# Performance work log

Hardware: AMD Instinct MI355X
Metric: run time of the kernel (lower is better)

## Reference

```python
import jax, jax.numpy as jnp
import numpy as np

D, U, NNZ, B = 8192, 4096, 1_700_000, 1024

def setup_inputs() -> dict:
    key = jax.random.key(0)
    k1, k2, k3, k4 = jax.random.split(key, 4)
    x = jax.random.normal(k1, (B, D), dtype=jnp.float32)
    kernel_vector = jax.random.normal(k2, (NNZ,), dtype=jnp.float32) * 0.02
    bias = jax.random.normal(k3, (U,), dtype=jnp.float32) * 0.01
    flat = jax.random.randint(k4, (NNZ,), 0, D * U)  # random sparsity pattern
    nonzero_ind = jnp.stack([flat // U, flat % U], axis=1).astype(jnp.int32)  # [NNZ, 2]
    return {"x": x, "kernel_vector": kernel_vector, "bias": bias, "nonzero_ind": nonzero_ind}

def reference(x, kernel_vector, bias, nonzero_ind):
    # scatter_nd: build dense (D, U) kernel from nonzero entries (duplicates add, as in tf.scatter_nd)
    W = jnp.zeros((D, U), dtype=kernel_vector.dtype).at[nonzero_ind[:, 0], nonzero_ind[:, 1]].add(kernel_vector)
    out = x @ W + bias  # [B, U]
    return jnp.tanh(out)
```

## Files before the change

kernel.cpp:

```cpp
#include <hip/hip_runtime.h>
#include <hip/hip_fp16.h>
#include <cmath>

#define DIM_M 1024
#define DIM_K 8192
#define DIM_N 4096
#define SPLIT 4
#define KSPL  (DIM_K / SPLIT)
#define BKT   64
#define NT    (KSPL / BKT)
#define NB    1024
#define EPB   8192
#define CVTB  1024

typedef __attribute__((ext_vector_type(8))) _Float16 half8;
typedef __attribute__((ext_vector_type(4))) float floatx4;

struct __align__(8) Half4 { __half2 a, b; };

__device__ inline void gload_lds16(const void* g, void* l) {
    __builtin_amdgcn_global_load_lds(
        (const __attribute__((address_space(1))) void*)g,
        (__attribute__((address_space(3))) void*)l, 16, 0, 0);
}

__global__ __launch_bounds__(512) void cluster_k(const int* __restrict__ ind,
                                                 const float* __restrict__ kv,
                                                 uint2* __restrict__ ebuf,
                                                 unsigned* __restrict__ ofs,
                                                 int nnz, int nblk,
                                                 const floatx4* __restrict__ xin,
                                                 Half4* __restrict__ xout) {
    extern __shared__ char csm[];
    const int tid = threadIdx.x;

    if (blockIdx.x >= nblk) {
        const int cb = blockIdx.x - nblk;
        const int base = cb * 2048;
        #pragma unroll
        for (int j = 0; j < 4; ++j) {
            int i = base + j * 512 + tid;
            floatx4 f = xin[i];
            Half4 h;
            h.a = __floats2half2_rn(f.x, f.y);
            h.b = __floats2half2_rn(f.z, f.w);
            xout[i] = h;
        }
        return;
    }

    uint2*    buf = (uint2*)csm;
    unsigned* cur = (unsigned*)(csm + 65536);
    unsigned* ss  = (unsigned*)(csm + 69632);
    const int blk = blockIdx.x;
    const int base = blk * EPB;
    const int lim = min(nnz - base, EPB);
    const int4*   ip = (const int4*)(ind + 2 * (size_t)base);
    const float2* vp = (const float2*)(kv + base);

    for (int i = tid; i < NB; i += 512) cur[i] = 0u;
    __syncthreads();
    for (int k2 = tid; k2 < lim / 2; k2 += 512) {
        int4 w = ip[k2];
        atomicAdd(&cur[w.y >> 2], 1u);
        atomicAdd(&cur[w.w >> 2], 1u);
    }
    if ((lim & 1) && tid == 0) {
        int u = ind[2 * (size_t)(base + lim - 1) + 1];
        atomicAdd(&cur[u >> 2], 1u);
    }
    __syncthreads();
    unsigned c0 = cur[2 * tid], c1 = cur[2 * tid + 1];
    unsigned own = c0 + c1;
    ss[tid] = own;
    __syncthreads();
    for (int off = 1; off < 512; off <<= 1) {
        unsigned t = (tid >= off) ? ss[tid - off] : 0u;
        __syncthreads();
        ss[tid] += t;
        __syncthreads();
    }
    unsigned e0 = ss[tid] - own;
    unsigned e1 = e0 + c0;
    __syncthreads();
    cur[2 * tid]     = e0;
    cur[2 * tid + 1] = e1;
    unsigned* obase = ofs + (size_t)blk * (NB + 1);
    obase[2 * tid]     = e0;
    obase[2 * tid + 1] = e1;
    if (tid == 511) obase[NB] = ss[511];
    __syncthreads();
    for (int k2 = tid; k2 < lim / 2; k2 += 512) {
        int4 w = ip[k2];
        float2 v = vp[k2];
        unsigned r0 = atomicAdd(&cur[w.y >> 2], 1u);
        buf[r0] = make_uint2(((unsigned)(w.y & 3) << 13) | (unsigned)w.x, __float_as_uint(v.x));
        unsigned r1 = atomicAdd(&cur[w.w >> 2], 1u);
        buf[r1] = make_uint2(((unsigned)(w.w & 3) << 13) | (unsigned)w.z, __float_as_uint(v.y));
    }
    if ((lim & 1) && tid == 0) {
        size_t e = (size_t)base + lim - 1;
        int d = ind[2 * e], u = ind[2 * e + 1];
        unsigned r = atomicAdd(&cur[u >> 2], 1u);
        buf[r] = make_uint2(((unsigned)(u & 3) << 13) | (unsigned)d, __float_as_uint(kv[e]));
    }
    __syncthreads();
    for (int j = tid; j < lim; j += 512)
        ebuf[(size_t)blk * EPB + j] = buf[j];
}

__global__ __launch_bounds__(512) void accum_k(const uint2* __restrict__ ebuf,
                                               const unsigned* __restrict__ ofs,
                                               int nblk,
                                               Half4* __restrict__ wh4) {
    extern __shared__ float reg[];
    floatx4* reg4 = (floatx4*)reg;
    const int tid = threadIdx.x, bin = blockIdx.x;
    for (int i = tid; i < 8192; i += 512) reg4[i] = floatx4{0.f, 0.f, 0.f, 0.f};
    __syncthreads();
    for (int s2 = tid; s2 < 2 * nblk; s2 += 512) {
        const int sb = s2 >> 1;
        const unsigned* ob = ofs + (size_t)sb * (NB + 1) + bin;
        unsigned o0 = ob[0] + (s2 & 1), o1 = ob[1];
        const uint2* p = ebuf + (size_t)sb * EPB;
        for (unsigned e = o0; e < o1; e += 2) {
            uint2 v = p[e];
            atomicAdd(&reg[v.x], __uint_as_float(v.y));
        }
    }
    __syncthreads();
    for (int i = tid; i < 8192; i += 512) {
        floatx4 f = reg4[i];
        Half4 h;
        h.a = __floats2half2_rn(f.x, f.y);
        h.b = __floats2half2_rn(f.z, f.w);
        wh4[(size_t)bin * 8192 + i] = h;
    }
}

__global__ __launch_bounds__(1024, 4) void gemm8_k(
    const _Float16* __restrict__ Ah,
    const _Float16* __restrict__ Bh,
    _Float16*       __restrict__ part)
{
    extern __shared__ char smem[];

    const int tid  = threadIdx.x;
    const int lane = tid & 63;
    const int wave = tid >> 6;

    const int bid = blockIdx.x;
    const int swz = (bid & 7) * 32 + (bid >> 3);
    const int n0  = (swz >> 4) * 256;
    const int rem = swz & 15;
    const int m0  = (rem >> 2) * 256;
    const int sp  = rem & 3;
    const size_t kbase = (size_t)sp * KSPL;

    const int srow = tid >> 3;
    const int sch  = (tid & 7) ^ (srow & 7);
    const _Float16* aSg = Ah + (size_t)(m0 + srow) * DIM_K + kbase + sch * 8;
    const _Float16* bSg = Bh + (size_t)(n0 + srow) * DIM_K + kbase + sch * 8;
    char* aLg = smem + wave * 1024;
    char* bLg = smem + 32768 + wave * 1024;

    const int wn  = wave & 3;
    const int wrm = wave >> 2;
    const int q   = lane >> 4;
    const int l7  = lane & 7;
    const char* aRd = smem + (wrm * 64 + (lane & 15)) * 128;
    const char* bRd = smem + 32768 + (wn * 64 + (lane & 15)) * 128;
    const int ch0 = ((0 * 4 + q) ^ l7) * 16;
    const int ch1 = ((1 * 4 + q) ^ l7) * 16;

    floatx4 acc[4][4] = {};
    half8 aF[4], bF[4];

#define STAGE(C)                                                              \
    { _Pragma("unroll") for (int p = 0; p < 2; ++p) {                         \
        gload_lds16(aSg + (size_t)p * (128 * DIM_K), aLg + (C) * 65536 + p * 16384); \
        gload_lds16(bSg + (size_t)p * (128 * DIM_K), bLg + (C) * 65536 + p * 16384); } \
      aSg += BKT; bSg += BKT; }

#define PH(C, CH)                                                             \
    { _Pragma("unroll") for (int i = 0; i < 4; ++i)                           \
        aF[i] = *(const half8*)(aRd + (C) * 65536 + i * 2048 + (CH));         \
      _Pragma("unroll") for (int i = 0; i < 4; ++i)                           \
        bF[i] = *(const half8*)(bRd + (C) * 65536 + i * 2048 + (CH));         \
      asm volatile("s_waitcnt lgkmcnt(0)" ::: "memory");                      \
      __builtin_amdgcn_sched_barrier(0);                                      \
      __builtin_amdgcn_s_setprio(1);                                          \
      _Pragma("unroll") for (int mi = 0; mi < 4; ++mi)                        \
        _Pragma("unroll") for (int ni = 0; ni < 4; ++ni)                      \
          acc[mi][ni] = __builtin_amdgcn_mfma_f32_16x16x32_f16(               \
              aF[mi], bF[ni], acc[mi][ni], 0, 0, 0);                          \
      __builtin_amdgcn_s_setprio(0); }

#define KTILE(C) PH(C, ch0) PH(C, ch1)

    STAGE(0)
    STAGE(1)
    asm volatile("s_waitcnt vmcnt(4)" ::: "memory");
    __builtin_amdgcn_s_barrier();

    for (int t2 = 0; t2 < NT / 2; ++t2) {
        KTILE(0)
        __builtin_amdgcn_s_barrier();
        if (t2 < NT / 2 - 1) {
            STAGE(0)
            asm volatile("s_waitcnt vmcnt(4)" ::: "memory");
        } else {
            asm volatile("s_waitcnt vmcnt(0)" ::: "memory");
        }
        __builtin_amdgcn_s_barrier();
        KTILE(1)
        if (t2 < NT / 2 - 1) {
            __builtin_amdgcn_s_barrier();
            STAGE(1)
            asm volatile("s_waitcnt vmcnt(4)" ::: "memory");
            __builtin_amdgcn_s_barrier();
        }
    }

#undef KTILE
#undef PH
#undef STAGE

    _Float16* pbase = part + (size_t)sp * DIM_M * DIM_N;
    #pragma unroll
    for (int ni = 0; ni < 4; ++ni) {
        const int col = n0 + wn * 64 + ni * 16 + (lane & 15);
        #pragma unroll
        for (int mi = 0; mi < 4; ++mi) {
            const int row = m0 + wrm * 64 + mi * 16 + (q << 2);
            #pragma unroll
            for (int r = 0; r < 4; ++r)
                pbase[(size_t)(row + r) * DIM_N + col] = (_Float16)acc[mi][ni][r];
        }
    }
}

__global__ void reduce_tanh(const Half4* __restrict__ part, const float* __restrict__ bias,
                            floatx4* __restrict__ out) {
    const int n4 = DIM_M * DIM_N / 4;
    int i = blockIdx.x * blockDim.x + threadIdx.x;
    if (i < n4) {
        float sx = 0.f, sy = 0.f, sz = 0.f, sw = 0.f;
        #pragma unroll
        for (int sp = 0; sp < SPLIT; ++sp) {
            Half4 p = part[(size_t)sp * n4 + i];
            float2 lo = __half22float2(p.a);
            float2 hi = __half22float2(p.b);
            sx += lo.x; sy += lo.y; sz += hi.x; sw += hi.y;
        }
        floatx4 b = ((const floatx4*)bias)[i & (DIM_N / 4 - 1)];
        floatx4 o;
        o.x = tanhf(sx + b.x);
        o.y = tanhf(sy + b.y);
        o.z = tanhf(sz + b.z);
        o.w = tanhf(sw + b.w);
        out[i] = o;
    }
}

extern "C" void kernel_launch(void* const* d_in, const int* in_sizes, int n_in,
                              void* d_out, int out_size, void* d_ws, size_t ws_size,
                              hipStream_t stream) {
    const float* x    = (const float*)d_in[0];
    const float* kv   = (const float*)d_in[1];
    const float* bias = (const float*)d_in[2];
    const int*   ind  = (const int*)d_in[3];
    float* out = (float*)d_out;
    const int nnz = in_sizes[1];

    char* ws = (char*)d_ws;
    _Float16* wh = (_Float16*)ws;
    const size_t whBytes = (size_t)DIM_N * DIM_K * 2;
    _Float16* xh = (_Float16*)(ws + whBytes);
    const size_t xhBytes = (size_t)DIM_M * DIM_K * 2;
    _Float16* part = (_Float16*)(ws + whBytes + xhBytes);
    const size_t partBytes = (size_t)SPLIT * DIM_M * DIM_N * 2;
    uint2* ebuf = (uint2*)(ws + whBytes + xhBytes + partBytes);
    const size_t ebufBytes = (size_t)16 << 20;
    unsigned* ofs = (unsigned*)(ws + whBytes + xhBytes + partBytes + ebufBytes);

    const int oN4 = DIM_M * DIM_N / 4;
    const int nblk = (nnz + EPB - 1) / EPB;

    hipFuncSetAttribute((const void*)cluster_k,
                        hipFuncAttributeMaxDynamicSharedMemorySize, 71680);
    cluster_k<<<nblk + CVTB, 512, 71680, stream>>>(ind, kv, ebuf, ofs, nnz, nblk,
                                                   (const floatx4*)x, (Half4*)xh);

    hipFuncSetAttribute((const void*)accum_k,
                        hipFuncAttributeMaxDynamicSharedMemorySize, 131072);
    accum_k<<<NB, 512, 131072, stream>>>(ebuf, ofs, nblk, (Half4*)wh);

    hipFuncSetAttribute((const void*)gemm8_k,
                        hipFuncAttributeMaxDynamicSharedMemorySize, 131072);
    gemm8_k<<<dim3(256), 1024, 131072, stream>>>(xh, wh, part);

    reduce_tanh<<<(oN4 + 255) / 256, 256, 0, stream>>>((const Half4*)part, bias, (floatx4*)out);
}
```

Measured before the change: 115.9 us.

## Load GEMM A operand directly to registers and triple-buffer B in LDS

The fp16 GEMM no longer stages the A tile through LDS. Each wave loads its A fragments straight from global memory into registers, double-buffered across half-k steps. Only B goes through LDS, now with a three-slot ring buffer and a single barrier per k-tile, and the LDS allocation drops to 96KB. The aim is to cut LDS traffic and barrier count and to overlap global loads with MFMA work. In exchange, A is read redundantly from global/L2 by the four waves sharing a row block, and synchronisation of the async B loads relies on implicit waits.

Result: slower. 217.6 us (+87.8%).

```diff
diff --git a/kernel.cpp b/kernel.cpp
--- a/kernel.cpp
+++ b/kernel.cpp
@@ -159,72 +159,70 @@
 
     const int srow = tid >> 3;
     const int sch  = (tid & 7) ^ (srow & 7);
-    const _Float16* aSg = Ah + (size_t)(m0 + srow) * DIM_K + kbase + sch * 8;
     const _Float16* bSg = Bh + (size_t)(n0 + srow) * DIM_K + kbase + sch * 8;
-    char* aLg = smem + wave * 1024;
-    char* bLg = smem + 32768 + wave * 1024;
+    const int sofs = wave * 1024;
 
     const int wn  = wave & 3;
     const int wrm = wave >> 2;
     const int q   = lane >> 4;
     const int l7  = lane & 7;
-    const char* aRd = smem + (wrm * 64 + (lane & 15)) * 128;
-    const char* bRd = smem + 32768 + (wn * 64 + (lane & 15)) * 128;
-    const int ch0 = ((0 * 4 + q) ^ l7) * 16;
-    const int ch1 = ((1 * 4 + q) ^ l7) * 16;
+    const int bRdOfs = (wn * 64 + (lane & 15)) * 128;
+    const int ch0 = (q ^ l7) * 16;
+    const int ch1 = ((4 + q) ^ l7) * 16;
+
+    const half8* aP = (const half8*)(Ah + (size_t)(m0 + wrm * 64 + (lane & 15)) * DIM_K
+                                     + kbase + q * 8);
 
     floatx4 acc[4][4] = {};
-    half8 aF[4], bF[4];
-
-#define STAGE(C)                                                              \
-    { _Pragma("unroll") for (int p = 0; p < 2; ++p) {                         \
-        gload_lds16(aSg + (size_t)p * (128 * DIM_K), aLg + (C) * 65536 + p * 16384); \
-        gload_lds16(bSg + (size_t)p * (128 * DIM_K), bLg + (C) * 65536 + p * 16384); } \
-      aSg += BKT; bSg += BKT; }
-
-#define PH(C, CH)                                                             \
+    half8 aFA[4], aFB[4], bF[4];
+
+#define STAGE2(SB)                                                            \
+    { gload_lds16(bSg,                        (SB) + sofs);                   \
+      gload_lds16(bSg + (size_t)128 * DIM_K,  (SB) + 16384 + sofs);           \
+      bSg += BKT; }
+
+#define LOADA(DST)                                                            \
     { _Pragma("unroll") for (int i = 0; i < 4; ++i)                           \
-        aF[i] = *(const half8*)(aRd + (C) * 65536 + i * 2048 + (CH));         \
-      _Pragma("unroll") for (int i = 0; i < 4; ++i)                           \
-        bF[i] = *(const half8*)(bRd + (C) * 65536 + i * 2048 + (CH));         \
-      asm volatile("s_waitcnt lgkmcnt(0)" ::: "memory");                      \
-      __builtin_amdgcn_sched_barrier(0);                                      \
-      __builtin_amdgcn_s_setprio(1);                                          \
-      _Pragma("unroll") for (int mi = 0; mi < 4; ++mi)                        \
+        DST[i] = aP[(size_t)i * 16384];                                       \
+      aP += 4; }
+
+#define RDB(CH)                                                               \
+    { _Pragma("unroll") for (int i = 0; i < 4; ++i)                           \
+        bF[i] = *(const half8*)(rb + bRdOfs + i * 2048 + (CH)); }
+
+#define MM(AU)                                                                \
+    __builtin_amdgcn_s_setprio(1);                                            \
+    { _Pragma("unroll") for (int mi = 0; mi < 4; ++mi)                        \
         _Pragma("unroll") for (int ni = 0; ni < 4; ++ni)                      \
           acc[mi][ni] = __builtin_amdgcn_mfma_f32_16x16x32_f16(               \
-              aF[mi], bF[ni], acc[mi][ni], 0, 0, 0);                          \
-      __builtin_amdgcn_s_setprio(0); }
-
-#define KTILE(C) PH(C, ch0) PH(C, ch1)
-
-    STAGE(0)
-    STAGE(1)
-    asm volatile("s_waitcnt vmcnt(4)" ::: "memory");
+              AU[mi], bF[ni], acc[mi][ni], 0, 0, 0); }                        \
+    __builtin_amdgcn_s_setprio(0);
+
+    char* rb = smem;
+    char* sb = smem + 2 * 32768;
+    STAGE2(smem)
+    STAGE2(smem + 32768)
+    LOADA(aFA)
+    asm volatile("s_waitcnt vmcnt(2)" ::: "memory");
     __builtin_amdgcn_s_barrier();
 
-    for (int t2 = 0; t2 < NT / 2; ++t2) {
-        KTILE(0)
+    for (int t = 0; t < NT; ++t) {
+        RDB(ch0)
+        STAGE2(sb)
+        LOADA(aFB)
+        MM(aFA)
+        RDB(ch1)
+        LOADA(aFA)
+        MM(aFB)
+        rb = (rb == smem + 2 * 32768) ? smem : rb + 32768;
+        sb = (sb == smem + 2 * 32768) ? smem : sb + 32768;
         __builtin_amdgcn_s_barrier();
-        if (t2 < NT / 2 - 1) {
-            STAGE(0)
-            asm volatile("s_waitcnt vmcnt(4)" ::: "memory");
-        } else {
-            asm volatile("s_waitcnt vmcnt(0)" ::: "memory");
-        }
-        __builtin_amdgcn_s_barrier();
-        KTILE(1)
-        if (t2 < NT / 2 - 1) {
-            __builtin_amdgcn_s_barrier();
-            STAGE(1)
-            asm volatile("s_waitcnt vmcnt(4)" ::: "memory");
-            __builtin_amdgcn_s_barrier();
-        }
-    }
-
-#undef KTILE
-#undef PH
-#undef STAGE
+    }
+
+#undef MM
+#undef RDB
+#undef LOADA
+#undef STAGE2
 
     _Float16* pbase = part + (size_t)sp * DIM_M * DIM_N;
     #pragma unroll
@@ -297,8 +295,8 @@
     accum_k<<<NB, 512, 131072, stream>>>(ebuf, ofs, nblk, (Half4*)wh);
 
     hipFuncSetAttribute((const void*)gemm8_k,
-                        hipFuncAttributeMaxDynamicSharedMemorySize, 131072);
-    gemm8_k<<<dim3(256), 1024, 131072, stream>>>(xh, wh, part);
+                        hipFuncAttributeMaxDynamicSharedMemorySize, 98304);
+    gemm8_k<<<dim3(256), 1024, 98304, stream>>>(xh, wh, part);
 
     reduce_tanh<<<(oN4 + 255) / 256, 256, 0, stream>>>((const Half4*)part, bias, (floatx4*)out);
 }
```
